# Kernel optimization log

Hardware: AMD Instinct MI355X
Metric: run time of the kernel (lower is better)

## Reference

```python
import jax, jax.numpy as jnp
import numpy as np
import math

ALPHA = 0.5
GAMMA_ALPHA = math.gamma(ALPHA)

def _xavier(key, fan_in, fan_out):
    limit = math.sqrt(6.0 / (fan_in + fan_out))
    return jax.random.uniform(key, (fan_in, fan_out), jnp.float32, -limit, limit)

def setup_inputs() -> dict:
    key = jax.random.key(0)
    ks = jax.random.split(key, 8)
    B, T, D_IN, H, D_OUT = 512, 1024, 64, 256, 64
    x = jax.random.normal(ks[0], (B, D_IN), jnp.float32)
    t = jnp.arange(T, dtype=jnp.float32) * 0.01  # increasing time grid
    W0 = _xavier(ks[1], D_IN + 1, H); b0 = jnp.zeros((H,), jnp.float32)
    W1 = _xavier(ks[2], H, H);        b1 = jnp.zeros((H,), jnp.float32)
    W2 = _xavier(ks[3], H, H);        b2 = jnp.zeros((H,), jnp.float32)
    W3 = _xavier(ks[4], H, D_OUT);    b3 = jnp.zeros((D_OUT,), jnp.float32)
    return {"x": x, "t": t, "W0": W0, "b0": b0, "W1": W1, "b1": b1,
            "W2": W2, "b2": b2, "W3": W3, "b3": b3}

def reference(x, t, W0, b0, W1, b1, W2, b2, W3, b3):
    # Fractional Euler: y_i = y_{i-1} + (dt^alpha / Gamma(alpha)) * tanh(MLP([t_{i-1}, y_{i-1}]))
    B = x.shape[0]
    y0 = x  # input_dim == output_dim, so initial state is x directly
    t_prev = t[:-1]            # [T-1]
    dt = t[1:] - t[:-1]        # [T-1]

    def mlp(tp, state):
        h = jnp.concatenate([jnp.full((B, 1), tp, dtype=state.dtype), state], axis=-1)
        h = h @ W0 + b0
        h = h @ W1 + b1  # nn.Sequential has no activations between linears
        h = h @ W2 + b2
        h = h @ W3 + b3
        return jnp.tanh(h)  # single tanh applied in ode_func

    def step(state, inputs):
        tp, d = inputs
        deriv = mlp(tp, state)
        factor = (d ** ALPHA) / GAMMA_ALPHA
        new = state + factor * deriv
        return new, new

    _, traj = jax.lax.scan(step, y0, (t_prev, dt))   # traj: [T-1, B, D_OUT]
    solution = jnp.concatenate([y0[:, None, :], jnp.swapaxes(traj, 0, 1)], axis=1)
    return solution  # [B, T, D_OUT]
```

## Files before the change

kernel.cpp:

```cpp
#include <hip/hip_runtime.h>
#include <math.h>

#define HDIM 256
#define DDIM 64
#define BROWS 512
#define TSTEPS 1024
#define AROWS 66

typedef float f32x2 __attribute__((ext_vector_type(2)));
typedef float f32x4 __attribute__((ext_vector_type(4)));

__global__ void compose1(const float* __restrict__ W0, const float* __restrict__ b0,
                         const float* __restrict__ W1, const float* __restrict__ b1,
                         float* __restrict__ out1) {
    int r = blockIdx.x;
    int c = threadIdx.x;
    const float* arow = (r < 65) ? (W0 + r * HDIM) : b0;
    float acc = (r == 65) ? b1[c] : 0.0f;
    for (int h = 0; h < HDIM; ++h)
        acc = fmaf(arow[h], W1[h * HDIM + c], acc);
    out1[r * HDIM + c] = acc;
}

__global__ void compose2(const float* __restrict__ in1,
                         const float* __restrict__ W2, const float* __restrict__ b2,
                         float* __restrict__ out2) {
    int r = blockIdx.x, c = threadIdx.x;
    const float* arow = in1 + r * HDIM;
    float acc = (r == 65) ? b2[c] : 0.0f;
    for (int h = 0; h < HDIM; ++h)
        acc = fmaf(arow[h], W2[h * HDIM + c], acc);
    out2[r * HDIM + c] = acc;
}

__global__ void compose3(const float* __restrict__ in2,
                         const float* __restrict__ W3, const float* __restrict__ b3,
                         float* __restrict__ out3) {
    int r = blockIdx.x, c = threadIdx.x;
    const float* arow = in2 + r * HDIM;
    float acc = (r == 65) ? b3[c] : 0.0f;
    for (int h = 0; h < HDIM; ++h)
        acc = fmaf(arow[h], W3[h * DDIM + c], acc);
    out3[r * DDIM + c] = acc;
}

__device__ __forceinline__ void pkfma(f32x2& acc, f32x2 a, f32x2 b) {
    asm("v_pk_fma_f32 %0, %1, %2, %0" : "+v"(acc) : "v"(a), "v"(b));
}

__launch_bounds__(64, 1)
__global__ void fode_scan(const float* __restrict__ x, const float* __restrict__ t,
                          const float* __restrict__ Weff,
                          float* __restrict__ out) {
    const int b = blockIdx.x;
    const int d = threadIdx.x;

    __shared__ float  ylds[DDIM];
    __shared__ float2 plds[TSTEPS];

    const float invG = 0.56418958354775628695f;

    for (int i = d; i < TSTEPS - 1; i += DDIM) {
        float t0 = t[i];
        float t1 = t[i + 1];
        plds[i] = make_float2(t0, sqrtf(t1 - t0) * invG);
    }

    f32x2 Wp[DDIM / 2];
#pragma unroll
    for (int c = 0; c < DDIM / 2; ++c) {
        Wp[c].x = Weff[(1 + 2 * c) * DDIM + d];
        Wp[c].y = Weff[(2 + 2 * c) * DDIM + d];
    }
    const float wt   = Weff[d];
    const float bias = Weff[65 * DDIM + d];

    float y = x[b * DDIM + d];
    float* op = out + (size_t)b * TSTEPS * DDIM + d;
    *op = y;
    ylds[d] = y;
    asm volatile("" ::: "memory");

    float2 prm = plds[0];

    for (int k = 0; k < TSTEPS - 1; ++k) {
        f32x4 yv[16];
#pragma unroll
        for (int c = 0; c < 16; ++c)
            yv[c] = *reinterpret_cast<const f32x4*>(&ylds[c * 4]);

        float2 prm_next = plds[k + 1];
        float base = fmaf(prm.x, wt, bias);

        f32x2 acc0 = {0.f, 0.f}, acc1 = {0.f, 0.f};
#pragma unroll
        for (int c = 0; c < 16; ++c) {
            f32x2 lo = __builtin_shufflevector(yv[c], yv[c], 0, 1);
            f32x2 hi = __builtin_shufflevector(yv[c], yv[c], 2, 3);
            pkfma(acc0, lo, Wp[2 * c + 0]);
            pkfma(acc1, hi, Wp[2 * c + 1]);
        }
        float s = ((acc0.x + acc0.y) + (acc1.x + acc1.y)) + base;

        float e  = __builtin_amdgcn_exp2f(s * 2.88539008177792681472f);
        float th = fmaf(-2.0f, __builtin_amdgcn_rcpf(e + 1.0f), 1.0f);

        y = fmaf(prm.y, th, y);

        ylds[d] = y;
        asm volatile("" ::: "memory");
        op += DDIM;
        *op = y;
        prm = prm_next;
    }
}

extern "C" void kernel_launch(void* const* d_in, const int* in_sizes, int n_in,
                              void* d_out, int out_size, void* d_ws, size_t ws_size,
                              hipStream_t stream) {
    const float* x  = (const float*)d_in[0];
    const float* t  = (const float*)d_in[1];
    const float* W0 = (const float*)d_in[2];
    const float* b0 = (const float*)d_in[3];
    const float* W1 = (const float*)d_in[4];
    const float* b1 = (const float*)d_in[5];
    const float* W2 = (const float*)d_in[6];
    const float* b2 = (const float*)d_in[7];
    const float* W3 = (const float*)d_in[8];
    const float* b3 = (const float*)d_in[9];
    float* out = (float*)d_out;

    float* buf1 = (float*)d_ws;
    float* buf2 = buf1 + AROWS * HDIM;
    float* buf3 = buf2 + AROWS * HDIM;

    compose1<<<AROWS, HDIM, 0, stream>>>(W0, b0, W1, b1, buf1);
    compose2<<<AROWS, HDIM, 0, stream>>>(buf1, W2, b2, buf2);
    compose3<<<AROWS, DDIM, 0, stream>>>(buf2, W3, b3, buf3);
    fode_scan<<<BROWS, DDIM, 0, stream>>>(x, t, buf3, out);
}
```

Baseline: 286.2 us.

## Replace LDS matvec broadcast with DPP/permlane exchange and incremental pre-activation update

The per-step matvec no longer goes through LDS. The scan now keeps the pre-activation s in registers and updates it incrementally as s += dt*wt + f*(C - 2*W·r), so only the reciprocal vector r has to be broadcast across lanes. That broadcast uses DPP moves plus permlane16/permlane32 swaps instead of an LDS store/barrier/load round trip. The weights are pre-scaled by the exp2 constant, and the time parameters are prefetched with inline ds_read. The aim is to shorten the serial dependency chain of each step, at the cost of more cross-lane instructions, and the incremental recurrence can change rounding behaviour.

```diff
diff --git a/kernel.cpp b/kernel.cpp
--- a/kernel.cpp
+++ b/kernel.cpp
@@ -8,7 +8,7 @@
 #define AROWS 66
 
 typedef float f32x2 __attribute__((ext_vector_type(2)));
-typedef float f32x4 __attribute__((ext_vector_type(4)));
+typedef int   i32x2 __attribute__((ext_vector_type(2)));
 
 __global__ void compose1(const float* __restrict__ W0, const float* __restrict__ b0,
                          const float* __restrict__ W1, const float* __restrict__ b1,
@@ -48,6 +48,27 @@
     asm("v_pk_fma_f32 %0, %1, %2, %0" : "+v"(acc) : "v"(a), "v"(b));
 }
 
+#define DPP_QP_XOR1 0xB1
+#define DPP_QP_XOR2 0x4E
+#define DPP_ROW_MIRROR 0x140
+#define DPP_ROW_HALF_MIRROR 0x141
+
+template <int CTRL>
+__device__ __forceinline__ unsigned dpp_mov(unsigned v) {
+    return (unsigned)__builtin_amdgcn_update_dpp(0, (int)v, CTRL, 0xF, 0xF, true);
+}
+
+__device__ __forceinline__ void gather16(unsigned v, unsigned bq[16]) {
+    bq[0] = v;
+    bq[1] = dpp_mov<DPP_QP_XOR1>(bq[0]);
+    bq[2] = dpp_mov<DPP_QP_XOR2>(bq[0]);
+    bq[3] = dpp_mov<DPP_QP_XOR2>(bq[1]);
+#pragma unroll
+    for (int i = 0; i < 4; ++i) bq[4 + i] = dpp_mov<DPP_ROW_HALF_MIRROR>(bq[i]);
+#pragma unroll
+    for (int i = 0; i < 8; ++i) bq[8 + i] = dpp_mov<DPP_ROW_MIRROR>(bq[i]);
+}
+
 __launch_bounds__(64, 1)
 __global__ void fode_scan(const float* __restrict__ x, const float* __restrict__ t,
                           const float* __restrict__ Weff,
@@ -55,64 +76,128 @@
     const int b = blockIdx.x;
     const int d = threadIdx.x;
 
-    __shared__ float  ylds[DDIM];
-    __shared__ float2 plds[TSTEPS];
+    __shared__ __align__(8) float2 plds[TSTEPS];
 
     const float invG = 0.56418958354775628695f;
+    const float K2L = 2.88539008177792681472f;
 
     for (int i = d; i < TSTEPS - 1; i += DDIM) {
         float t0 = t[i];
         float t1 = t[i + 1];
-        plds[i] = make_float2(t0, sqrtf(t1 - t0) * invG);
-    }
-
-    f32x2 Wp[DDIM / 2];
-#pragma unroll
-    for (int c = 0; c < DDIM / 2; ++c) {
-        Wp[c].x = Weff[(1 + 2 * c) * DDIM + d];
-        Wp[c].y = Weff[(2 + 2 * c) * DDIM + d];
-    }
-    const float wt   = Weff[d];
-    const float bias = Weff[65 * DDIM + d];
+        float dt = t1 - t0;
+        plds[i] = make_float2(dt, sqrtf(dt) * invG);
+    }
+
+    const int lo = d & 31;
+    const int hh = d >> 5;
+
+    int sx[16], sy[16];
+    {
+        unsigned bq[16];
+        gather16((unsigned)d, bq);
+#pragma unroll
+        for (int i = 0; i < 16; ++i) {
+            i32x2 s = __builtin_amdgcn_permlane16_swap((int)bq[i], (int)bq[i],
+                                                       false, false);
+            sx[i] = s.x;
+            sy[i] = s.y;
+        }
+    }
+
+    f32x2 WaP[16], WbP[16];
+#pragma unroll
+    for (int c = 0; c < 16; ++c) {
+        WaP[c].x = -2.0f * K2L * Weff[(1 + sx[c]) * DDIM + lo];
+        WaP[c].y = -2.0f * K2L * Weff[(1 + sy[c]) * DDIM + lo];
+        WbP[c].x = -2.0f * K2L * Weff[(1 + sx[c]) * DDIM + lo + 32];
+        WbP[c].y = -2.0f * K2L * Weff[(1 + sy[c]) * DDIM + lo + 32];
+    }
+    const float wts   = K2L * Weff[d];
+    const float biass = K2L * Weff[65 * DDIM + d];
+    float Cd = 0.0f;
+    for (int j = 0; j < DDIM; ++j) Cd += Weff[(1 + j) * DDIM + d];
+    Cd *= K2L;
+
+    auto cal = __builtin_amdgcn_permlane32_swap(d, d, false, false);
+    const bool pick0 = (cal[0] == (d ^ 32));
+
+    const unsigned pbase = (unsigned)(uintptr_t)&plds[0];
+    const float t0g = t[0];
 
     float y = x[b * DDIM + d];
     float* op = out + (size_t)b * TSTEPS * DDIM + d;
     *op = y;
-    ylds[d] = y;
-    asm volatile("" ::: "memory");
-
-    float2 prm = plds[0];
+
+#define DOT32(VIN, DOTOUT)                                                   \
+    {                                                                        \
+        unsigned bq[16];                                                     \
+        gather16(__float_as_uint(VIN), bq);                                  \
+        f32x2 P[16];                                                         \
+        _Pragma("unroll")                                                    \
+        for (int i = 0; i < 16; ++i) {                                       \
+            i32x2 sw_ = __builtin_amdgcn_permlane16_swap((int)bq[i],         \
+                                                    (int)bq[i], false, false);\
+            P[i].x = __int_as_float(sw_.x);                                  \
+            P[i].y = __int_as_float(sw_.y);                                  \
+        }                                                                    \
+        f32x2 accA0 = {0.f, 0.f}, accA1 = {0.f, 0.f};                        \
+        f32x2 accB0 = {0.f, 0.f}, accB1 = {0.f, 0.f};                        \
+        _Pragma("unroll")                                                    \
+        for (int c = 0; c < 16; c += 2) {                                    \
+            pkfma(accA0, P[c], WaP[c]);                                      \
+            pkfma(accB0, P[c], WbP[c]);                                      \
+            pkfma(accA1, P[c + 1], WaP[c + 1]);                              \
+            pkfma(accB1, P[c + 1], WbP[c + 1]);                              \
+        }                                                                    \
+        f32x2 ra = accA0 + accA1;                                            \
+        f32x2 rb = accB0 + accB1;                                            \
+        float qa = ra.x + ra.y;                                              \
+        float qb = rb.x + rb.y;                                              \
+        float keep = (d < 32) ? qa : qb;                                     \
+        float send = (d < 32) ? qb : qa;                                     \
+        auto sw2 = __builtin_amdgcn_permlane32_swap(__float_as_int(send),    \
+                                               __float_as_int(send), false, false);\
+        float recv = __int_as_float(pick0 ? sw2[0] : sw2[1]);                \
+        DOTOUT = keep + recv;                                                \
+    }
+
+    float s;
+    {
+        asm volatile("s_waitcnt lgkmcnt(0)" ::: "memory");
+        float dotY;
+        DOT32(y, dotY);
+        s = fmaf(-0.5f, dotY, fmaf(t0g, wts, biass));
+    }
+
+    f32x2 prm;
+    prm.x = plds[0].x;
+    prm.y = plds[0].y;
 
     for (int k = 0; k < TSTEPS - 1; ++k) {
-        f32x4 yv[16];
-#pragma unroll
-        for (int c = 0; c < 16; ++c)
-            yv[c] = *reinterpret_cast<const f32x4*>(&ylds[c * 4]);
-
-        float2 prm_next = plds[k + 1];
-        float base = fmaf(prm.x, wt, bias);
-
-        f32x2 acc0 = {0.f, 0.f}, acc1 = {0.f, 0.f};
-#pragma unroll
-        for (int c = 0; c < 16; ++c) {
-            f32x2 lo = __builtin_shufflevector(yv[c], yv[c], 0, 1);
-            f32x2 hi = __builtin_shufflevector(yv[c], yv[c], 2, 3);
-            pkfma(acc0, lo, Wp[2 * c + 0]);
-            pkfma(acc1, hi, Wp[2 * c + 1]);
-        }
-        float s = ((acc0.x + acc0.y) + (acc1.x + acc1.y)) + base;
-
-        float e  = __builtin_amdgcn_exp2f(s * 2.88539008177792681472f);
-        float th = fmaf(-2.0f, __builtin_amdgcn_rcpf(e + 1.0f), 1.0f);
-
-        y = fmaf(prm.y, th, y);
-
-        ylds[d] = y;
-        asm volatile("" ::: "memory");
+        f32x2 prmn;
+        unsigned paddr = pbase + 8u * (unsigned)(k + 1);
+        asm volatile("ds_read_b64 %0, %1" : "=&v"(prmn) : "v"(paddr));
+
+        float dt = prm.x, f = prm.y;
+        float sc  = fmaf(f, Cd, fmaf(dt, wts, s));
+        float yf  = y + f;
+        float m2f = -2.0f * f;
+
+        float e = __builtin_amdgcn_exp2f(s);
+        float r = __builtin_amdgcn_rcpf(e + 1.0f);
+
+        float dotT;
+        DOT32(r, dotT);
+        s = fmaf(f, dotT, sc);
+
+        y = fmaf(m2f, r, yf);
         op += DDIM;
         *op = y;
-        prm = prm_next;
-    }
+
+        asm volatile("s_waitcnt lgkmcnt(0)" ::: "memory");
+        prm = prmn;
+    }
+#undef DOT32
 }
 
 extern "C" void kernel_launch(void* const* d_in, const int* in_sizes, int n_in,
```

Result: slower. 323.1 us (+12.9%).
